# Kernel tuning notes

Measured on AMD Instinct MI355X. Metric: run time of the kernel, lower is better.

The kernel has to match this reference:

```python
import jax, jax.numpy as jnp
import numpy as np

B, N, E, H = 2, 2048, 256, 8
D = E // H  # head dim = 32


def setup_inputs() -> dict:
    key = jax.random.key(0)
    ks = jax.random.split(key, 8)
    query_bbox = jax.random.uniform(ks[0], (B, N, 4), dtype=jnp.float32)
    query_feat = jax.random.normal(ks[1], (B, N, E), dtype=jnp.float32)
    s = 1.0 / np.sqrt(E)
    in_proj_w = jax.random.uniform(ks[2], (3 * E, E), minval=-s, maxval=s, dtype=jnp.float32)
    in_proj_b = jax.random.uniform(ks[3], (3 * E,), minval=-s, maxval=s, dtype=jnp.float32)
    out_proj_w = jax.random.uniform(ks[4], (E, E), minval=-s, maxval=s, dtype=jnp.float32)
    out_proj_b = jnp.zeros((E,), dtype=jnp.float32)
    # init_weights(): gen_tau weight zeroed, bias ~ U(0, 2)
    tau_w = jnp.zeros((H, E), dtype=jnp.float32)
    tau_b = jax.random.uniform(ks[5], (H,), minval=0.0, maxval=2.0, dtype=jnp.float32)
    return {
        "query_bbox": query_bbox,
        "query_feat": query_feat,
        "in_proj_w": in_proj_w,
        "in_proj_b": in_proj_b,
        "out_proj_w": out_proj_w,
        "out_proj_b": out_proj_b,
        "tau_w": tau_w,
        "tau_b": tau_b,
    }


def reference(query_bbox, query_feat, in_proj_w, in_proj_b, out_proj_w, out_proj_b, tau_w, tau_b):
    # pairwise center distances, negated; computed under no_grad in torch
    centers = query_bbox[..., :2]                                  # [B,N,2]
    diff = centers[:, :, None, :] - centers[:, None, :, :]         # [B,N,N,2]
    dist = -jnp.sqrt(jnp.sum(diff * diff, axis=-1))                # [B,N,N]
    dist = jax.lax.stop_gradient(dist)

    # per-head tau from query features
    tau = query_feat @ tau_w.T + tau_b                             # [B,N,H]
    tau = jnp.transpose(tau, (0, 2, 1))                            # [B,H,N]
    attn_mask = dist[:, None, :, :] * tau[..., None]               # [B,H,N,N]

    # multi-head self-attention (q = k = v = query_feat)
    qkv = query_feat @ in_proj_w.T + in_proj_b                     # [B,N,3E]
    q, k, v = jnp.split(qkv, 3, axis=-1)
    def heads(x):
        return jnp.transpose(x.reshape(B, N, H, D), (0, 2, 1, 3))  # [B,H,N,D]
    q, k, v = heads(q), heads(k), heads(v)

    scores = jnp.einsum("bhid,bhjd->bhij", q, k) / jnp.sqrt(jnp.float32(D))
    scores = scores + attn_mask
    attn = jax.nn.softmax(scores, axis=-1)                         # [B,H,N,N]
    o = jnp.einsum("bhij,bhjd->bhid", attn, v)                     # [B,H,N,D]
    o = jnp.transpose(o, (0, 2, 1, 3)).reshape(B, N, E)
    out = o @ out_proj_w.T + out_proj_b

    # mmcv MultiheadAttention adds the identity (residual); dropout in eval = id
    return query_feat + out
```

## Files before the change

kernel.cpp:

```cpp
#include <hip/hip_runtime.h>
#include <math.h>

#define BB 2
#define NN 2048
#define EE 256
#define HH 8
#define DD 32

typedef __attribute__((ext_vector_type(8))) short short8;
typedef __attribute__((ext_vector_type(4))) float f32x4;

__device__ inline unsigned short f2bf(float f) {
  union { float f; unsigned int u; } a; a.f = f;
  unsigned int r = a.u + 0x7FFFu + ((a.u >> 16) & 1u);
  return (unsigned short)(r >> 16);
}
__device__ inline float bf2f(short s) {
  union { unsigned int u; float f; } a;
  a.u = ((unsigned int)(unsigned short)s) << 16;
  return a.f;
}

__global__ __launch_bounds__(256) void prep_kernel(const float* __restrict__ bbox,
                                                   const float* __restrict__ feat,
                                                   const float* __restrict__ in_w,
                                                   const float* __restrict__ out_w,
                                                   const float* __restrict__ tau_w,
                                                   const float* __restrict__ tau_b,
                                                   unsigned short* __restrict__ in_wb,
                                                   unsigned short* __restrict__ out_wb,
                                                   float* __restrict__ tau2,
                                                   unsigned short* __restrict__ featb,
                                                   unsigned short* __restrict__ nds) {
  int blk = blockIdx.x;
  int tid = threadIdx.x;
  if (blk < 256) {
    int i = blk * 256 + tid;
    float4 v;
    unsigned short* dst;
    if (i < 49152) {
      v = ((const float4*)in_w)[i];
      dst = in_wb + (size_t)i * 4;
    } else {
      v = ((const float4*)out_w)[i - 49152];
      dst = out_wb + (size_t)(i - 49152) * 4;
    }
    ushort4 u;
    u.x = f2bf(v.x); u.y = f2bf(v.y); u.z = f2bf(v.z); u.w = f2bf(v.w);
    *(ushort4*)dst = u;
  } else if (blk < 384) {
    int idx = (blk - 256) * 256 + tid;
    int row = idx >> 3, h = idx & 7;
    const float4* f = (const float4*)(feat + (size_t)row * EE);
    const float4* w = (const float4*)(tau_w + (size_t)h * EE);
    float s = 0.f;
#pragma unroll 8
    for (int e = 0; e < EE / 4; ++e) {
      float4 a = f[e], b4 = w[e];
      s = fmaf(a.x, b4.x, s);
      s = fmaf(a.y, b4.y, s);
      s = fmaf(a.z, b4.z, s);
      s = fmaf(a.w, b4.w, s);
      if ((e >> 3) == h) {
        ushort4 u;
        u.x = f2bf(a.x); u.y = f2bf(a.y); u.z = f2bf(a.z); u.w = f2bf(a.w);
        *(ushort4*)(featb + (size_t)row * EE + e * 4) = u;
      }
    }
    tau2[idx] = (s + tau_b[h]) * 1.4426950408889634f;
  } else {
    int blk2 = blk - 384;
    int bq = blk2 >> 3;
    int yy = blk2 & 7;
    int b = bq >> 7, qt = bq & 127;
    int w = tid >> 6, lane = tid & 63;
    int q15 = lane & 15, g = lane >> 4;
    int jt = yy * 4 + w;

    const float* bi = bbox + (size_t)(b * NN + qt * 16 + q15) * 4;
    float cix = bi[0], ciy = bi[1];
    const float* bj = bbox + (size_t)(b * NN + jt * 64) * 4;

    float nd[16];
#pragma unroll
    for (int t = 0; t < 4; ++t) {
#pragma unroll
      for (int r = 0; r < 4; ++r) {
        int j = t * 16 + g * 4 + r;
        float2 cj = *(const float2*)(bj + (size_t)j * 4);
        float dx = cix - cj.x, dy = ciy - cj.y;
        nd[t * 4 + r] = -__builtin_amdgcn_sqrtf(fmaf(dy, dy, dx * dx));
      }
    }
    unsigned int u[8];
#pragma unroll
    for (int i = 0; i < 8; ++i)
      asm("v_cvt_pk_bf16_f32 %0, %1, %2" : "=v"(u[i]) : "v"(nd[2 * i]), "v"(nd[2 * i + 1]));
    unsigned short* dst = nds + ((size_t)(b * 128 + qt) * 32 + jt) * 1024 + lane * 16;
    *(uint4*)dst = make_uint4(u[0], u[1], u[2], u[3]);
    *(uint4*)(dst + 8) = make_uint4(u[4], u[5], u[6], u[7]);
  }
}

template <int MODE>
__global__ __launch_bounds__(256) void gemm_mfma_kernel(const unsigned short* __restrict__ Ab,
                                                        const unsigned short* __restrict__ Wb,
                                                        const float* __restrict__ bias,
                                                        const float* __restrict__ resid,
                                                        float* __restrict__ Cf,
                                                        unsigned short* __restrict__ qb,
                                                        unsigned short* __restrict__ kh,
                                                        unsigned short* __restrict__ vpi) {
  int tid = threadIdx.x;
  int wv = tid >> 6, lane = tid & 63;
  int p = lane & 15, g = lane >> 4;
  int mW = blockIdx.y * 64 + wv * 16;
  int nB = blockIdx.x * 64;

  const unsigned short* ap = Ab + (size_t)(mW + p) * 256 + g * 8;
  const unsigned short* wp = Wb + (size_t)(nB + p) * 256 + g * 8;

  f32x4 acc[4] = {{0.f, 0.f, 0.f, 0.f}, {0.f, 0.f, 0.f, 0.f},
                  {0.f, 0.f, 0.f, 0.f}, {0.f, 0.f, 0.f, 0.f}};
#pragma unroll
  for (int kk = 0; kk < 8; ++kk) {
    short8 af = *(const short8*)(ap + kk * 32);
#pragma unroll
    for (int t = 0; t < 4; ++t) {
      short8 wf = *(const short8*)(wp + (size_t)t * 16 * 256 + kk * 32);
      acc[t] = __builtin_amdgcn_mfma_f32_16x16x32_bf16(af, wf, acc[t], 0, 0, 0);
    }
  }

#pragma unroll
  for (int t = 0; t < 4; ++t) {
    int n = nB + t * 16 + p;
    float bn = bias[n];
#pragma unroll
    for (int r = 0; r < 4; ++r) {
      int m = mW + g * 4 + r;
      float v = acc[t][r] + bn;
      if (MODE == 1) {
        Cf[(size_t)m * 256 + n] = v + resid[(size_t)m * 256 + n];
      } else {
        int b = m >> 11, tok = m & 2047;
        if (n < 256) {
          qb[(size_t)m * 256 + n] = f2bf(v * 0.25506659272582955f);
        } else if (n < 512) {
          int h = (n - 256) >> 5, d = n & 31;
          kh[((size_t)(b * 8 + h) * NN + tok) * 32 + d] = f2bf(v);
        } else {
          int h = (n - 512) >> 5, d = n & 31;
          int cp = ((tok & 15) << 1) | ((tok >> 4) & 1);
          vpi[(((size_t)(b * 8 + h) * 64 + (tok >> 5)) * 32 + d) * 32 + cp] = f2bf(v);
        }
      }
    }
  }
}

__global__ __launch_bounds__(256) void attn_kernel(const unsigned short* __restrict__ qb,
                                                   const unsigned short* __restrict__ kh,
                                                   const unsigned short* __restrict__ vpi,
                                                   const unsigned short* __restrict__ nds,
                                                   const float* __restrict__ tau2,
                                                   unsigned short* __restrict__ ob) {
  __shared__ float accT[4][32][17];
  __shared__ float lT[4][16];
  __shared__ float linv[16];

  int bh = blockIdx.x;
  int b = bh >> 3, h = bh & 7;
  int qtb = blockIdx.y;
  int tid = threadIdx.x;
  int w = tid >> 6;
  int lane = tid & 63;
  int q15 = lane & 15, g = lane >> 4;
  int rowq = b * NN + qtb * 16 + q15;

  short8 qf = *(const short8*)(qb + (size_t)rowq * 256 + h * 32 + g * 8);
  float t2 = tau2[(size_t)rowq * HH + h];

  float l = 0.f;
  f32x4 acc0 = {0.f, 0.f, 0.f, 0.f}, acc1 = {0.f, 0.f, 0.f, 0.f};

  const unsigned short* kb = kh + (size_t)bh * NN * 32 + q15 * 32 + g * 8;
  const unsigned short* vb = vpi + (size_t)bh * NN * 32 + q15 * 32 + g * 8;
  const unsigned short* ndb = nds + (size_t)(b * 128 + qtb) * 32768 + lane * 16;

  int j0base = w * 512;

  short8 kf[2][4];
  short8 vf[2][2][2];
  short8 nf[2][2];

#pragma unroll
  for (int t = 0; t < 4; ++t)
    kf[0][t] = *(const short8*)(kb + (size_t)(j0base + t * 16) * 32);
#pragma unroll
  for (int t2i = 0; t2i < 2; ++t2i)
#pragma unroll
    for (int dh = 0; dh < 2; ++dh)
      vf[0][t2i][dh] = *(const short8*)(vb + (size_t)((j0base >> 5) + t2i) * 1024 + dh * 512);
  nf[0][0] = *(const short8*)(ndb + (size_t)(j0base >> 6) * 1024);
  nf[0][1] = *(const short8*)(ndb + (size_t)(j0base >> 6) * 1024 + 8);

#pragma unroll
  for (int tt = 0; tt < 8; ++tt) {
    const int cur = tt & 1, nxt = cur ^ 1;
    const int j0 = j0base + tt * 64;
    if (tt < 7) {
      const int j1 = j0 + 64;
#pragma unroll
      for (int t = 0; t < 4; ++t)
        kf[nxt][t] = *(const short8*)(kb + (size_t)(j1 + t * 16) * 32);
#pragma unroll
      for (int t2i = 0; t2i < 2; ++t2i)
#pragma unroll
        for (int dh = 0; dh < 2; ++dh)
          vf[nxt][t2i][dh] = *(const short8*)(vb + (size_t)((j1 >> 5) + t2i) * 1024 + dh * 512);
      nf[nxt][0] = *(const short8*)(ndb + (size_t)(j1 >> 6) * 1024);
      nf[nxt][1] = *(const short8*)(ndb + (size_t)(j1 >> 6) * 1024 + 8);
    }
    f32x4 st[4];
#pragma unroll
    for (int t = 0; t < 4; ++t)
      st[t] = __builtin_amdgcn_mfma_f32_16x16x32_bf16(kf[cur][t], qf, (f32x4){0.f, 0.f, 0.f, 0.f}, 0, 0, 0);
    float p[16], lsum = 0.f;
#pragma unroll
    for (int i = 0; i < 16; ++i) {
      float ndf = bf2f(i < 8 ? nf[cur][0][i] : nf[cur][1][i - 8]);
      float e = fminf(fmaf(ndf, t2, st[i >> 2][i & 3]), 30.f);
      p[i] = __builtin_amdgcn_exp2f(e);
      lsum += p[i];
    }
    l += lsum;
    union { short8 v; unsigned int u[4]; } pf[2];
#pragma unroll
    for (int t2i = 0; t2i < 2; ++t2i)
#pragma unroll
      for (int wq = 0; wq < 4; ++wq) {
        asm("v_cvt_pk_bf16_f32 %0, %1, %2"
            : "=v"(pf[t2i].u[wq]) : "v"(p[t2i * 8 + wq]), "v"(p[t2i * 8 + 4 + wq]));
      }
    acc0 = __builtin_amdgcn_mfma_f32_16x16x32_bf16(vf[cur][0][0], pf[0].v, acc0, 0, 0, 0);
    acc1 = __builtin_amdgcn_mfma_f32_16x16x32_bf16(vf[cur][0][1], pf[0].v, acc1, 0, 0, 0);
    acc0 = __builtin_amdgcn_mfma_f32_16x16x32_bf16(vf[cur][1][0], pf[1].v, acc0, 0, 0, 0);
    acc1 = __builtin_amdgcn_mfma_f32_16x16x32_bf16(vf[cur][1][1], pf[1].v, acc1, 0, 0, 0);
  }

  l += __shfl_xor(l, 16);
  l += __shfl_xor(l, 32);

#pragma unroll
  for (int r = 0; r < 4; ++r) {
    accT[w][g * 4 + r][q15] = acc0[r];
    accT[w][16 + g * 4 + r][q15] = acc1[r];
  }
  if (g == 0) lT[w][q15] = l;
  __syncthreads();

  if (tid < 16) {
    float L = lT[0][tid] + lT[1][tid] + lT[2][tid] + lT[3][tid];
    linv[tid] = 1.f / fmaxf(L, 1e-30f);
  }
  __syncthreads();

#pragma unroll
  for (int ii = 0; ii < 2; ++ii) {
    int i = tid + ii * 256;
    int q = i >> 5, d = i & 31;
    float ov = (accT[0][d][q] + accT[1][d][q] + accT[2][d][q] + accT[3][d][q]) * linv[q];
    ob[((size_t)b * NN + qtb * 16 + q) * EE + h * 32 + d] = f2bf(ov);
  }
}

extern "C" void kernel_launch(void* const* d_in, const int* in_sizes, int n_in,
                              void* d_out, int out_size, void* d_ws, size_t ws_size,
                              hipStream_t stream) {
  const float* bbox  = (const float*)d_in[0];
  const float* feat  = (const float*)d_in[1];
  const float* in_w  = (const float*)d_in[2];
  const float* in_b  = (const float*)d_in[3];
  const float* out_w = (const float*)d_in[4];
  const float* out_b = (const float*)d_in[5];
  const float* tau_w = (const float*)d_in[6];
  const float* tau_b = (const float*)d_in[7];
  float* out = (float*)d_out;

  unsigned short* ob     = (unsigned short*)d_ws;
  unsigned short* featb  = ob + 1048576;
  unsigned short* qb     = featb + 1048576;
  unsigned short* kh     = qb + 1048576;
  unsigned short* vpi    = kh + 1048576;
  unsigned short* in_wb  = vpi + 1048576;
  unsigned short* out_wb = in_wb + 196608;
  float* tau2 = (float*)(out_wb + 65536);
  unsigned short* nds = (unsigned short*)(tau2 + 32768);

  prep_kernel<<<dim3(2432), 256, 0, stream>>>(bbox, feat, in_w, out_w, tau_w, tau_b,
                                              in_wb, out_wb, tau2, featb, nds);
  gemm_mfma_kernel<0><<<dim3(12, 64), 256, 0, stream>>>(featb, in_wb, in_b, nullptr, nullptr,
                                                        qb, kh, vpi);
  attn_kernel<<<dim3(BB * HH, NN / 16), 256, 0, stream>>>(qb, kh, vpi, nds, tau2, ob);
  gemm_mfma_kernel<1><<<dim3(4, 64), 256, 0, stream>>>(ob, out_wb, out_b, feat, out,
                                                       nullptr, nullptr, nullptr);
}
```

Before: 90.28 us.

## Compute distance tiles inside attention and share them across heads via LDS

The pairwise distance matrix is no longer precomputed into a global bf16 buffer in the prep kernel. Each attention block now covers one 16-query tile for all 8 heads, one wave per head, and computes each 64-key distance tile once per block into double-buffered shared memory that every head reads. Each wave walks the full key range itself, so the cross-wave split of the KV range and its shared-memory reduction go away. The cost is a __syncthreads per key tile and only 256 blocks of 512 threads. Each wave's key loop is now serial and four times longer, which cuts parallelism across the GPU.

```diff
diff --git a/kernel.cpp b/kernel.cpp
--- a/kernel.cpp
+++ b/kernel.cpp
@@ -21,8 +21,7 @@
   return a.f;
 }
 
-__global__ __launch_bounds__(256) void prep_kernel(const float* __restrict__ bbox,
-                                                   const float* __restrict__ feat,
+__global__ __launch_bounds__(256) void prep_kernel(const float* __restrict__ feat,
                                                    const float* __restrict__ in_w,
                                                    const float* __restrict__ out_w,
                                                    const float* __restrict__ tau_w,
@@ -30,8 +29,7 @@
                                                    unsigned short* __restrict__ in_wb,
                                                    unsigned short* __restrict__ out_wb,
                                                    float* __restrict__ tau2,
-                                                   unsigned short* __restrict__ featb,
-                                                   unsigned short* __restrict__ nds) {
+                                                   unsigned short* __restrict__ featb) {
   int blk = blockIdx.x;
   int tid = threadIdx.x;
   if (blk < 256) {
@@ -48,7 +46,7 @@
     ushort4 u;
     u.x = f2bf(v.x); u.y = f2bf(v.y); u.z = f2bf(v.z); u.w = f2bf(v.w);
     *(ushort4*)dst = u;
-  } else if (blk < 384) {
+  } else {
     int idx = (blk - 256) * 256 + tid;
     int row = idx >> 3, h = idx & 7;
     const float4* f = (const float4*)(feat + (size_t)row * EE);
@@ -68,37 +66,6 @@
       }
     }
     tau2[idx] = (s + tau_b[h]) * 1.4426950408889634f;
-  } else {
-    int blk2 = blk - 384;
-    int bq = blk2 >> 3;
-    int yy = blk2 & 7;
-    int b = bq >> 7, qt = bq & 127;
-    int w = tid >> 6, lane = tid & 63;
-    int q15 = lane & 15, g = lane >> 4;
-    int jt = yy * 4 + w;
-
-    const float* bi = bbox + (size_t)(b * NN + qt * 16 + q15) * 4;
-    float cix = bi[0], ciy = bi[1];
-    const float* bj = bbox + (size_t)(b * NN + jt * 64) * 4;
-
-    float nd[16];
-#pragma unroll
-    for (int t = 0; t < 4; ++t) {
-#pragma unroll
-      for (int r = 0; r < 4; ++r) {
-        int j = t * 16 + g * 4 + r;
-        float2 cj = *(const float2*)(bj + (size_t)j * 4);
-        float dx = cix - cj.x, dy = ciy - cj.y;
-        nd[t * 4 + r] = -__builtin_amdgcn_sqrtf(fmaf(dy, dy, dx * dx));
-      }
-    }
-    unsigned int u[8];
-#pragma unroll
-    for (int i = 0; i < 8; ++i)
-      asm("v_cvt_pk_bf16_f32 %0, %1, %2" : "=v"(u[i]) : "v"(nd[2 * i]), "v"(nd[2 * i + 1]));
-    unsigned short* dst = nds + ((size_t)(b * 128 + qt) * 32 + jt) * 1024 + lane * 16;
-    *(uint4*)dst = make_uint4(u[0], u[1], u[2], u[3]);
-    *(uint4*)(dst + 8) = make_uint4(u[4], u[5], u[6], u[7]);
   }
 }
 
@@ -159,120 +126,133 @@
   }
 }
 
-__global__ __launch_bounds__(256) void attn_kernel(const unsigned short* __restrict__ qb,
+__global__ __launch_bounds__(512) void attn_kernel(const unsigned short* __restrict__ qb,
                                                    const unsigned short* __restrict__ kh,
                                                    const unsigned short* __restrict__ vpi,
-                                                   const unsigned short* __restrict__ nds,
+                                                   const float* __restrict__ bbox,
                                                    const float* __restrict__ tau2,
                                                    unsigned short* __restrict__ ob) {
-  __shared__ float accT[4][32][17];
-  __shared__ float lT[4][16];
-  __shared__ float linv[16];
-
-  int bh = blockIdx.x;
-  int b = bh >> 3, h = bh & 7;
-  int qtb = blockIdx.y;
+  __shared__ unsigned int ndL[2][512];
+
+  int bq = blockIdx.x;
+  int b = bq >> 7, qt = bq & 127;
   int tid = threadIdx.x;
-  int w = tid >> 6;
+  int h = tid >> 6;
   int lane = tid & 63;
   int q15 = lane & 15, g = lane >> 4;
-  int rowq = b * NN + qtb * 16 + q15;
+  int rowq = b * NN + qt * 16 + q15;
+  int bh = b * 8 + h;
 
   short8 qf = *(const short8*)(qb + (size_t)rowq * 256 + h * 32 + g * 8);
   float t2 = tau2[(size_t)rowq * HH + h];
 
+  int lp = tid >> 3;
+  int ii = (tid * 2) & 15;
+  int qs = lp & 15, gs = lp >> 4;
+  int joff = (ii >> 2) * 16 + gs * 4 + (ii & 3);
+  const float* bq_ptr = bbox + (size_t)(b * NN + qt * 16 + qs) * 4;
+  float cix = bq_ptr[0], ciy = bq_ptr[1];
+  const float* bj_base = bbox + (size_t)b * NN * 4;
+
   float l = 0.f;
   f32x4 acc0 = {0.f, 0.f, 0.f, 0.f}, acc1 = {0.f, 0.f, 0.f, 0.f};
 
   const unsigned short* kb = kh + (size_t)bh * NN * 32 + q15 * 32 + g * 8;
   const unsigned short* vb = vpi + (size_t)bh * NN * 32 + q15 * 32 + g * 8;
-  const unsigned short* ndb = nds + (size_t)(b * 128 + qtb) * 32768 + lane * 16;
-
-  int j0base = w * 512;
-
-  short8 kf[2][4];
-  short8 vf[2][2][2];
-  short8 nf[2][2];
+
+  short8 kf0[4], kf1[4];
+  short8 vf0[2][2], vf1[2][2];
+
+#define STAGE_ND(buf, jj)                                                     \
+  {                                                                           \
+    int j = (jj) * 64 + joff;                                                 \
+    float2 c0 = *(const float2*)(bj_base + (size_t)j * 4);                    \
+    float2 c1 = *(const float2*)(bj_base + (size_t)(j + 1) * 4);              \
+    float dx0 = cix - c0.x, dy0 = ciy - c0.y;                                 \
+    float dx1 = cix - c1.x, dy1 = ciy - c1.y;                                 \
+    float d0 = -__builtin_amdgcn_sqrtf(fmaf(dy0, dy0, dx0 * dx0));            \
+    float d1 = -__builtin_amdgcn_sqrtf(fmaf(dy1, dy1, dx1 * dx1));            \
+    unsigned int u;                                                           \
+    asm("v_cvt_pk_bf16_f32 %0, %1, %2" : "=v"(u) : "v"(d0), "v"(d1));         \
+    ndL[buf][tid] = u;                                                        \
+  }
+
+#define TILE_BODY(CUR, TT)                                                    \
+  {                                                                           \
+    const int j0 = (TT) * 64;                                                 \
+    if ((TT) < 31) {                                                          \
+      STAGE_ND(CUR ^ 1, (TT) + 1);                                            \
+      const int j1 = j0 + 64;                                                 \
+      short8* kfn = (CUR) ? kf0 : kf1;                                        \
+      _Pragma("unroll") for (int t = 0; t < 4; ++t)                           \
+          kfn[t] = *(const short8*)(kb + (size_t)(j1 + t * 16) * 32);         \
+      _Pragma("unroll") for (int t2i = 0; t2i < 2; ++t2i)                     \
+          _Pragma("unroll") for (int dh = 0; dh < 2; ++dh)                    \
+          ((CUR) ? vf0 : vf1)[t2i][dh] =                                      \
+              *(const short8*)(vb + (size_t)((j1 >> 5) + t2i) * 1024 + dh * 512); \
+    }                                                                         \
+    short8* kfc = (CUR) ? kf1 : kf0;                                          \
+    f32x4 st[4];                                                              \
+    _Pragma("unroll") for (int t = 0; t < 4; ++t)                             \
+        st[t] = __builtin_amdgcn_mfma_f32_16x16x32_bf16(                      \
+            kfc[t], qf, (f32x4){0.f, 0.f, 0.f, 0.f}, 0, 0, 0);                \
+    const short8* ndp = (const short8*)((const unsigned short*)ndL[CUR] + lane * 16); \
+    short8 n0 = ndp[0];                                                       \
+    short8 n1 = ndp[1];                                                       \
+    float p[16], lsum = 0.f;                                                  \
+    _Pragma("unroll") for (int i = 0; i < 16; ++i) {                          \
+      float ndf = bf2f(i < 8 ? n0[i] : n1[i - 8]);                            \
+      float e = fminf(fmaf(ndf, t2, st[i >> 2][i & 3]), 30.f);                \
+      p[i] = __builtin_amdgcn_exp2f(e);                                       \
+      lsum += p[i];                                                           \
+    }                                                                         \
+    l += lsum;                                                                \
+    union { short8 v; unsigned int u[4]; } pf[2];                             \
+    _Pragma("unroll") for (int t2i = 0; t2i < 2; ++t2i)                       \
+        _Pragma("unroll") for (int wq = 0; wq < 4; ++wq) {                    \
+      asm("v_cvt_pk_bf16_f32 %0, %1, %2"                                      \
+          : "=v"(pf[t2i].u[wq])                                               \
+          : "v"(p[t2i * 8 + wq]), "v"(p[t2i * 8 + 4 + wq]));                  \
+    }                                                                         \
+    const short8(*vfc)[2] = (CUR) ? vf1 : vf0;                                \
+    acc0 = __builtin_amdgcn_mfma_f32_16x16x32_bf16(vfc[0][0], pf[0].v, acc0, 0, 0, 0); \
+    acc1 = __builtin_amdgcn_mfma_f32_16x16x32_bf16(vfc[0][1], pf[0].v, acc1, 0, 0, 0); \
+    acc0 = __builtin_amdgcn_mfma_f32_16x16x32_bf16(vfc[1][0], pf[1].v, acc0, 0, 0, 0); \
+    acc1 = __builtin_amdgcn_mfma_f32_16x16x32_bf16(vfc[1][1], pf[1].v, acc1, 0, 0, 0); \
+    __syncthreads();                                                          \
+  }
 
 #pragma unroll
   for (int t = 0; t < 4; ++t)
-    kf[0][t] = *(const short8*)(kb + (size_t)(j0base + t * 16) * 32);
+    kf0[t] = *(const short8*)(kb + (size_t)(t * 16) * 32);
 #pragma unroll
   for (int t2i = 0; t2i < 2; ++t2i)
 #pragma unroll
     for (int dh = 0; dh < 2; ++dh)
-      vf[0][t2i][dh] = *(const short8*)(vb + (size_t)((j0base >> 5) + t2i) * 1024 + dh * 512);
-  nf[0][0] = *(const short8*)(ndb + (size_t)(j0base >> 6) * 1024);
-  nf[0][1] = *(const short8*)(ndb + (size_t)(j0base >> 6) * 1024 + 8);
-
-#pragma unroll
-  for (int tt = 0; tt < 8; ++tt) {
-    const int cur = tt & 1, nxt = cur ^ 1;
-    const int j0 = j0base + tt * 64;
-    if (tt < 7) {
-      const int j1 = j0 + 64;
-#pragma unroll
-      for (int t = 0; t < 4; ++t)
-        kf[nxt][t] = *(const short8*)(kb + (size_t)(j1 + t * 16) * 32);
-#pragma unroll
-      for (int t2i = 0; t2i < 2; ++t2i)
-#pragma unroll
-        for (int dh = 0; dh < 2; ++dh)
-          vf[nxt][t2i][dh] = *(const short8*)(vb + (size_t)((j1 >> 5) + t2i) * 1024 + dh * 512);
-      nf[nxt][0] = *(const short8*)(ndb + (size_t)(j1 >> 6) * 1024);
-      nf[nxt][1] = *(const short8*)(ndb + (size_t)(j1 >> 6) * 1024 + 8);
-    }
-    f32x4 st[4];
-#pragma unroll
-    for (int t = 0; t < 4; ++t)
-      st[t] = __builtin_amdgcn_mfma_f32_16x16x32_bf16(kf[cur][t], qf, (f32x4){0.f, 0.f, 0.f, 0.f}, 0, 0, 0);
-    float p[16], lsum = 0.f;
-#pragma unroll
-    for (int i = 0; i < 16; ++i) {
-      float ndf = bf2f(i < 8 ? nf[cur][0][i] : nf[cur][1][i - 8]);
-      float e = fminf(fmaf(ndf, t2, st[i >> 2][i & 3]), 30.f);
-      p[i] = __builtin_amdgcn_exp2f(e);
-      lsum += p[i];
-    }
-    l += lsum;
-    union { short8 v; unsigned int u[4]; } pf[2];
-#pragma unroll
-    for (int t2i = 0; t2i < 2; ++t2i)
-#pragma unroll
-      for (int wq = 0; wq < 4; ++wq) {
-        asm("v_cvt_pk_bf16_f32 %0, %1, %2"
-            : "=v"(pf[t2i].u[wq]) : "v"(p[t2i * 8 + wq]), "v"(p[t2i * 8 + 4 + wq]));
-      }
-    acc0 = __builtin_amdgcn_mfma_f32_16x16x32_bf16(vf[cur][0][0], pf[0].v, acc0, 0, 0, 0);
-    acc1 = __builtin_amdgcn_mfma_f32_16x16x32_bf16(vf[cur][0][1], pf[0].v, acc1, 0, 0, 0);
-    acc0 = __builtin_amdgcn_mfma_f32_16x16x32_bf16(vf[cur][1][0], pf[1].v, acc0, 0, 0, 0);
-    acc1 = __builtin_amdgcn_mfma_f32_16x16x32_bf16(vf[cur][1][1], pf[1].v, acc1, 0, 0, 0);
+      vf0[t2i][dh] = *(const short8*)(vb + (size_t)t2i * 1024 + dh * 512);
+  STAGE_ND(0, 0);
+  __syncthreads();
+
+  for (int tt = 0; tt < 32; tt += 2) {
+    TILE_BODY(0, tt);
+    TILE_BODY(1, tt + 1);
   }
 
   l += __shfl_xor(l, 16);
   l += __shfl_xor(l, 32);
-
-#pragma unroll
-  for (int r = 0; r < 4; ++r) {
-    accT[w][g * 4 + r][q15] = acc0[r];
-    accT[w][16 + g * 4 + r][q15] = acc1[r];
-  }
-  if (g == 0) lT[w][q15] = l;
-  __syncthreads();
-
-  if (tid < 16) {
-    float L = lT[0][tid] + lT[1][tid] + lT[2][tid] + lT[3][tid];
-    linv[tid] = 1.f / fmaxf(L, 1e-30f);
-  }
-  __syncthreads();
-
-#pragma unroll
-  for (int ii = 0; ii < 2; ++ii) {
-    int i = tid + ii * 256;
-    int q = i >> 5, d = i & 31;
-    float ov = (accT[0][d][q] + accT[1][d][q] + accT[2][d][q] + accT[3][d][q]) * linv[q];
-    ob[((size_t)b * NN + qtb * 16 + q) * EE + h * 32 + d] = f2bf(ov);
-  }
+  float linv = 1.f / fmaxf(l, 1e-30f);
+
+  float o0[4], o1[4];
+#pragma unroll
+  for (int r = 0; r < 4; ++r) { o0[r] = acc0[r] * linv; o1[r] = acc1[r] * linv; }
+  unsigned int w0[2], w1[2];
+  asm("v_cvt_pk_bf16_f32 %0, %1, %2" : "=v"(w0[0]) : "v"(o0[0]), "v"(o0[1]));
+  asm("v_cvt_pk_bf16_f32 %0, %1, %2" : "=v"(w0[1]) : "v"(o0[2]), "v"(o0[3]));
+  asm("v_cvt_pk_bf16_f32 %0, %1, %2" : "=v"(w1[0]) : "v"(o1[0]), "v"(o1[1]));
+  asm("v_cvt_pk_bf16_f32 %0, %1, %2" : "=v"(w1[1]) : "v"(o1[2]), "v"(o1[3]));
+  unsigned short* op = ob + (size_t)rowq * EE + h * 32;
+  *(uint2*)(op + g * 4) = make_uint2(w0[0], w0[1]);
+  *(uint2*)(op + 16 + g * 4) = make_uint2(w1[0], w1[1]);
 }
 
 extern "C" void kernel_launch(void* const* d_in, const int* in_sizes, int n_in,
@@ -296,13 +276,12 @@
   unsigned short* in_wb  = vpi + 1048576;
   unsigned short* out_wb = in_wb + 196608;
   float* tau2 = (float*)(out_wb + 65536);
-  unsigned short* nds = (unsigned short*)(tau2 + 32768);
-
-  prep_kernel<<<dim3(2432), 256, 0, stream>>>(bbox, feat, in_w, out_w, tau_w, tau_b,
-                                              in_wb, out_wb, tau2, featb, nds);
+
+  prep_kernel<<<dim3(384), 256, 0, stream>>>(feat, in_w, out_w, tau_w, tau_b,
+                                             in_wb, out_wb, tau2, featb);
   gemm_mfma_kernel<0><<<dim3(12, 64), 256, 0, stream>>>(featb, in_wb, in_b, nullptr, nullptr,
                                                         qb, kh, vpi);
-  attn_kernel<<<dim3(BB * HH, NN / 16), 256, 0, stream>>>(qb, kh, vpi, nds, tau2, ob);
+  attn_kernel<<<dim3(BB * 128), 512, 0, stream>>>(qb, kh, vpi, bbox, tau2, ob);
   gemm_mfma_kernel<1><<<dim3(4, 64), 256, 0, stream>>>(ob, out_wb, out_b, feat, out,
                                                        nullptr, nullptr, nullptr);
 }
```

Measured after the change: 89.86 us. No clear change (-0.5%).
